# Optimization experiments

Hardware: AMD Instinct MI355X
Metric: run time of the kernel (lower is better)

Reference implementation:

```python
import jax, jax.numpy as jnp
import numpy as np

D_MODEL = 4096
N_HEADS = 32
N_KV_HEADS = 8
HEAD_DIM = D_MODEL // N_HEADS  # 128
SEQ = 2048
BATCH = 1
ROPE_BASE = 10000.0


def build_rope_cache(max_seq_len, head_dim, base=10000.0):
    half = head_dim // 2
    pos = jnp.arange(max_seq_len, dtype=jnp.float32)
    inv_freqs = 1.0 / (base ** (jnp.arange(half, dtype=jnp.float32) / half))
    angles = pos[:, None] * inv_freqs[None, :]  # (S, half)
    return jnp.cos(angles), jnp.sin(angles)


def apply_rope(t, cos, sin):
    # t: (B, H, S, D); cos/sin: (S, D//2) broadcast over batch & heads.
    t_even = t[..., 0::2]
    t_odd = t[..., 1::2]
    c = cos[None, None, :, :]
    s = sin[None, None, :, :]
    rot_even = t_even * c - t_odd * s
    rot_odd = t_even * s + t_odd * c
    # interleave back into even/odd slots
    return jnp.stack([rot_even, rot_odd], axis=-1).reshape(t.shape)


def setup_inputs() -> dict:
    key = jax.random.key(0)
    kx, kq, kk, kv, ko = jax.random.split(key, 5)
    bound = 1.0 / np.sqrt(D_MODEL)
    x = jax.random.normal(kx, (BATCH, SEQ, D_MODEL), dtype=jnp.float32)
    # torch Linear weights: (out_features, in_features)
    wq = jax.random.uniform(kq, (N_HEADS * HEAD_DIM, D_MODEL), minval=-bound, maxval=bound, dtype=jnp.float32)
    wk = jax.random.uniform(kk, (N_KV_HEADS * HEAD_DIM, D_MODEL), minval=-bound, maxval=bound, dtype=jnp.float32)
    wv = jax.random.uniform(kv, (N_KV_HEADS * HEAD_DIM, D_MODEL), minval=-bound, maxval=bound, dtype=jnp.float32)
    wo = jax.random.uniform(ko, (D_MODEL, D_MODEL), minval=-bound, maxval=bound, dtype=jnp.float32)
    attn_mask = jnp.tril(jnp.ones((SEQ, SEQ), dtype=jnp.int32))[None, None, :, :]
    return {"x": x, "wq": wq, "wk": wk, "wv": wv, "wo": wo, "attn_mask": attn_mask}


def reference(x, wq, wk, wv, wo, attn_mask):
    B, S, _ = x.shape
    cos, sin = build_rope_cache(SEQ, HEAD_DIM, ROPE_BASE)
    cos, sin = cos[:S], sin[:S]
    q = (x @ wq.T).reshape(B, S, N_HEADS, HEAD_DIM).transpose(0, 2, 1, 3)      # (B,H,S,D)
    k = (x @ wk.T).reshape(B, S, N_KV_HEADS, HEAD_DIM).transpose(0, 2, 1, 3)   # (B,Hkv,S,D)
    v = (x @ wv.T).reshape(B, S, N_KV_HEADS, HEAD_DIM).transpose(0, 2, 1, 3)
    q = apply_rope(q, cos, sin)
    k = apply_rope(k, cos, sin)
    n_rep = N_HEADS // N_KV_HEADS
    if n_rep > 1:
        k = jnp.repeat(k, n_rep, axis=1)
        v = jnp.repeat(v, n_rep, axis=1)
    scores = jnp.einsum('bhqd,bhkd->bhqk', q, k) / jnp.sqrt(jnp.float32(HEAD_DIM))
    scores = jnp.where(attn_mask == 0, -jnp.inf, scores)
    attn = jax.nn.softmax(scores, axis=-1)
    out = jnp.einsum('bhqk,bhkd->bhqd', attn, v)
    out = out.transpose(0, 2, 1, 3).reshape(B, S, D_MODEL)
    return out @ wo.T
```

## Files before the change

kernel.cpp:

```cpp
#include <hip/hip_runtime.h>
#include <hip/hip_bf16.h>

typedef float f32x4 __attribute__((ext_vector_type(4)));
typedef __bf16 bf16x4 __attribute__((ext_vector_type(4)));
typedef __bf16 bf16x8 __attribute__((ext_vector_type(8)));

__device__ __forceinline__ void gld_lds16(const void* g, void* l) {
  __builtin_amdgcn_global_load_lds((const __attribute__((address_space(1))) void*)g,
                                   (__attribute__((address_space(3))) void*)l, 16, 0, 0);
}

__global__ void cvt_f32_bf16(const float* __restrict__ in, __bf16* __restrict__ out,
                             int n8) {
  int idx = blockIdx.x * blockDim.x + threadIdx.x;
  if (idx >= n8) return;
  f32x4 a = *(const f32x4*)(in + (size_t)idx * 8);
  f32x4 b = *(const f32x4*)(in + (size_t)idx * 8 + 4);
  bf16x8 o;
#pragma unroll
  for (int j = 0; j < 4; ++j) { o[j] = (__bf16)a[j]; o[4 + j] = (__bf16)b[j]; }
  *(bf16x8*)(out + (size_t)idx * 8) = o;
}

__global__ void build_trig(float* __restrict__ trig) {
  int idx = blockIdx.x * blockDim.x + threadIdx.x;
  if (idx >= 2048 * 64) return;
  int i = idx & 63, s = idx >> 6;
  float ang = (float)s * powf(10000.0f, -(float)i * (1.0f / 64.0f));
  float sn, cs;
  sincosf(ang, &sn, &cs);
  trig[idx * 2] = cs;
  trig[idx * 2 + 1] = sn;
}

__global__ void rope_bf16(__bf16* __restrict__ T, const float* __restrict__ trig,
                          int stride, int nh_mask, int nh_shift, float mul, int total) {
  int idx = blockIdx.x * blockDim.x + threadIdx.x;
  if (idx >= total) return;
  int i = idx & 63;
  int h = (idx >> 6) & nh_mask;
  int s = idx >> (6 + nh_shift);
  float cs = trig[(s * 64 + i) * 2];
  float sn = trig[(s * 64 + i) * 2 + 1];
  __bf16* p = T + (size_t)s * stride + h * 128 + 2 * i;
  float e = (float)p[0], o = (float)p[1];
  p[0] = (__bf16)((e * cs - o * sn) * mul);
  p[1] = (__bf16)((e * sn + o * cs) * mul);
}

__global__ __launch_bounds__(256) void transpose_v(const __bf16* __restrict__ KVb,
                                                   __bf16* __restrict__ Vt) {
  __shared__ __bf16 T[64][72];
  const int tid = threadIdx.x;
  const int s0 = blockIdx.x * 64, d0 = blockIdx.y * 64;
  const int r = tid >> 3, c8 = (tid & 7) * 8;
#pragma unroll
  for (int i = 0; i < 2; ++i) {
    int row = i * 32 + r;
    *(bf16x8*)&T[row][c8] = *(const bf16x8*)&KVb[(size_t)(s0 + row) * 2048 + 1024 + d0 + c8];
  }
  __syncthreads();
#pragma unroll
  for (int i = 0; i < 2; ++i) {
    int drow = i * 32 + r;
    bf16x8 o;
#pragma unroll
    for (int j = 0; j < 8; ++j) o[j] = T[c8 + j][drow];
    *(bf16x8*)&Vt[(size_t)(d0 + drow) * 2048 + s0 + c8] = o;
  }
}

template <int BM, int BN, typename OutT>
__global__ __launch_bounds__(256) void gemm_bf16(const __bf16* __restrict__ A,
                                                 const __bf16* __restrict__ B0,
                                                 const __bf16* __restrict__ B1,
                                                 int Nsplit, OutT* __restrict__ C,
                                                 int M, int N, int K) {
  constexpr int MI = BM / 32, NJ = BN / 32;
  constexpr int RA = BM / 32, RB = BN / 32;
  __shared__ __bf16 As[BM * 64] __attribute__((aligned(16)));
  __shared__ __bf16 Bs[BN * 64] __attribute__((aligned(16)));

  const int tid = threadIdx.x;
  const int lane = tid & 63;
  const int w = tid >> 6;
  const int nwg = gridDim.x * gridDim.y;
  const int orig = blockIdx.y * gridDim.x + blockIdx.x;
  const int wgid = (orig & 7) * (nwg >> 3) + (orig >> 3);
  const int m0 = (wgid % gridDim.x) * BM;
  const int n0 = (wgid / gridDim.x) * BN;
  const int li = lane & 15, lg = lane >> 4;

  const __bf16* bsrc[RB];
#pragma unroll
  for (int i = 0; i < RB; ++i) {
    int slot = i * 256 + w * 64 + lane;
    int row = slot >> 3;
    int sch = (slot & 7) ^ (row & 7);
    int n = n0 + row;
    bsrc[i] = (n < Nsplit ? B0 + (size_t)n * K : B1 + (size_t)(n - Nsplit) * K) +
              sch * 8;
  }
  const __bf16* asrc[RA];
#pragma unroll
  for (int i = 0; i < RA; ++i) {
    int slot = i * 256 + w * 64 + lane;
    int row = slot >> 3;
    int sch = (slot & 7) ^ (row & 7);
    asrc[i] = A + (size_t)(m0 + row) * K + sch * 8;
  }

  const int wr = (w >> 1) * (BM / 2);
  const int wc = (w & 1) * (BN / 2);

  f32x4 acc[MI][NJ] = {};

  for (int k0 = 0; k0 < K; k0 += 64) {
    __syncthreads();
#pragma unroll
    for (int i = 0; i < RA; ++i)
      gld_lds16(asrc[i] + k0, &As[(i * 256 + w * 64) * 8]);
#pragma unroll
    for (int i = 0; i < RB; ++i)
      gld_lds16(bsrc[i] + k0, &Bs[(i * 256 + w * 64) * 8]);
    __syncthreads();

#pragma unroll
    for (int u = 0; u < 2; ++u) {
      bf16x8 af[MI], bfr[NJ];
#pragma unroll
      for (int mi = 0; mi < MI; ++mi)
        af[mi] = *(const bf16x8*)&As[(wr + mi * 16 + li) * 64 +
                                     (((u * 4 + lg) ^ (li & 7)) * 8)];
#pragma unroll
      for (int nj = 0; nj < NJ; ++nj)
        bfr[nj] = *(const bf16x8*)&Bs[(wc + nj * 16 + li) * 64 +
                                      (((u * 4 + lg) ^ (li & 7)) * 8)];
#pragma unroll
      for (int mi = 0; mi < MI; ++mi)
#pragma unroll
        for (int nj = 0; nj < NJ; ++nj)
          acc[mi][nj] = __builtin_amdgcn_mfma_f32_16x16x32_bf16(af[mi], bfr[nj],
                                                                acc[mi][nj], 0, 0, 0);
    }
  }

  const int crow = lg * 4;
#pragma unroll
  for (int mi = 0; mi < MI; ++mi)
#pragma unroll
    for (int nj = 0; nj < NJ; ++nj)
#pragma unroll
      for (int r = 0; r < 4; ++r)
        C[(size_t)(m0 + wr + mi * 16 + crow + r) * N + (n0 + wc + nj * 16 + li)] =
            (OutT)acc[mi][nj][r];
}

__global__ __launch_bounds__(256) void attn_fwd_v5(const __bf16* __restrict__ Q,
                                                   const __bf16* __restrict__ KVb,
                                                   const __bf16* __restrict__ Vt,
                                                   __bf16* __restrict__ O) {
  const int tid = threadIdx.x;
  const int lane = tid & 63;
  const int w = tid >> 6;
  const int orig = blockIdx.x;
  const int chunk = orig & 7;
  const int wkk = orig >> 3;
  const int h = chunk * 4 + (wkk & 3);
  const int pair = wkk >> 2;
  const int kvh = h >> 2;

  __shared__ __bf16 Ks[2][64 * 128] __attribute__((aligned(16)));
  __shared__ __bf16 Vts[128 * 64] __attribute__((aligned(16)));
  __shared__ __bf16 Ps[4][32 * 72] __attribute__((aligned(16)));

  const int li = lane & 15, lg = lane >> 4;

  auto stage_k = [&](int k0, int buf) {
#pragma unroll
    for (int i = 0; i < 4; ++i) {
      int slot = i * 256 + tid;
      int row = slot >> 4;
      int sch = (slot & 15) ^ (row & 7);
      gld_lds16(&KVb[(size_t)(k0 + row) * 2048 + kvh * 128 + sch * 8],
                &Ks[buf][(i * 256 + w * 64) * 8]);
    }
  };
  auto stage_v = [&](int k0) {
#pragma unroll
    for (int i = 0; i < 4; ++i) {
      int slot = i * 256 + tid;
      int row = slot >> 3;
      int sch = (slot & 7) ^ (row & 7);
      gld_lds16(&Vt[(size_t)(kvh * 128 + row) * 2048 + k0 + sch * 8],
                &Vts[(i * 256 + w * 64) * 8]);
    }
  };

#pragma unroll 1
  for (int pass = 0; pass < 2; ++pass) {
    const int m0 = ((pass == 0) ? (15 - pair) : pair) * 128;
    const int rbase = m0 + w * 32;

    bf16x8 qf[2][4];
#pragma unroll
    for (int mt = 0; mt < 2; ++mt) {
      const __bf16* qrow = Q + (size_t)(rbase + mt * 16 + li) * 4096 + h * 128;
#pragma unroll
      for (int kc = 0; kc < 4; ++kc) qf[mt][kc] = *(const bf16x8*)(qrow + kc * 32 + lg * 8);
    }

    f32x4 accO[2][8] = {};
    float plane[2] = {0.f, 0.f};

    const int wmax = rbase + 31;
    const int ntile = (m0 + 128) >> 6;

    stage_k(0, 0);

#pragma unroll 1
    for (int t = 0; t < ntile; ++t) {
      const int k0 = t * 64;
      const int cur = t & 1;
      stage_v(k0);
      stage_k(t + 1 < ntile ? k0 + 64 : 0, cur ^ 1);

      asm volatile("s_waitcnt vmcnt(8)" ::: "memory");
      __builtin_amdgcn_s_barrier();
      __builtin_amdgcn_sched_barrier(0);
      asm volatile("" ::: "memory");

      const bool active = (k0 <= wmax);
      bf16x8 pa[2][2];
      if (active) {
        f32x4 s2[4][2] = {};
        __builtin_amdgcn_s_setprio(1);
#pragma unroll
        for (int nt = 0; nt < 4; ++nt)
#pragma unroll
          for (int kc = 0; kc < 4; ++kc) {
            bf16x8 kf = *(const bf16x8*)&Ks[cur][(li + 16 * nt) * 128 +
                                                (((4 * kc + lg) ^ (li & 7)) * 8)];
            s2[nt][0] = __builtin_amdgcn_mfma_f32_16x16x32_bf16(kf, qf[0][kc], s2[nt][0], 0, 0, 0);
            s2[nt][1] = __builtin_amdgcn_mfma_f32_16x16x32_bf16(kf, qf[1][kc], s2[nt][1], 0, 0, 0);
          }
        __builtin_amdgcn_s_setprio(0);

#pragma unroll
        for (int mt = 0; mt < 2; ++mt) {
          const int qb = rbase + mt * 16;
          const int q = qb + li;
          const bool needmask = (k0 + 63 > qb);
#pragma unroll
          for (int nt = 0; nt < 4; ++nt) {
            bf16x4 pk;
#pragma unroll
            for (int r = 0; r < 4; ++r) {
              const int key = k0 + 16 * nt + lg * 4 + r;
              float v = s2[nt][mt][r];
              if (needmask && key > q) v = -INFINITY;
              float p = exp2f(v);
              plane[mt] += p;
              pk[r] = (__bf16)p;
            }
            *(bf16x4*)&Ps[w][(mt * 16 + li) * 72 + 16 * nt + lg * 4] = pk;
          }
          pa[mt][0] = *(const bf16x8*)&Ps[w][(mt * 16 + li) * 72 + lg * 8];
          pa[mt][1] = *(const bf16x8*)&Ps[w][(mt * 16 + li) * 72 + 32 + lg * 8];
        }
      }

      asm volatile("s_waitcnt vmcnt(4)" ::: "memory");
      __builtin_amdgcn_s_barrier();
      __builtin_amdgcn_sched_barrier(0);
      asm volatile("" ::: "memory");

      if (active) {
        __builtin_amdgcn_s_setprio(1);
#pragma unroll
        for (int dt = 0; dt < 8; ++dt)
#pragma unroll
          for (int kc = 0; kc < 2; ++kc) {
            bf16x8 vf = *(const bf16x8*)&Vts[(li + 16 * dt) * 64 +
                                             (((4 * kc + lg) ^ (li & 7)) * 8)];
            accO[0][dt] = __builtin_amdgcn_mfma_f32_16x16x32_bf16(pa[0][kc], vf, accO[0][dt], 0, 0, 0);
            accO[1][dt] = __builtin_amdgcn_mfma_f32_16x16x32_bf16(pa[1][kc], vf, accO[1][dt], 0, 0, 0);
          }
        __builtin_amdgcn_s_setprio(0);
      }

      __builtin_amdgcn_s_barrier();
      __builtin_amdgcn_sched_barrier(0);
      asm volatile("" ::: "memory");
    }

#pragma unroll
    for (int mt = 0; mt < 2; ++mt) {
      float sum = plane[mt];
      sum += __shfl_xor(sum, 16);
      sum += __shfl_xor(sum, 32);
      float inv[4];
#pragma unroll
      for (int r = 0; r < 4; ++r) inv[r] = 1.0f / __shfl(sum, lg * 4 + r);
#pragma unroll
      for (int dt = 0; dt < 8; ++dt)
#pragma unroll
        for (int r = 0; r < 4; ++r)
          O[(size_t)(rbase + mt * 16 + lg * 4 + r) * 4096 + h * 128 + dt * 16 + li] =
              (__bf16)(accO[mt][dt][r] * inv[r]);
    }
  }
}

extern "C" void kernel_launch(void* const* d_in, const int* in_sizes, int n_in,
                              void* d_out, int out_size, void* d_ws, size_t ws_size,
                              hipStream_t stream) {
  const float* x  = (const float*)d_in[0];
  const float* wq = (const float*)d_in[1];
  const float* wk = (const float*)d_in[2];
  const float* wv = (const float*)d_in[3];
  const float* wo = (const float*)d_in[4];
  float* out = (float*)d_out;

  const int S = 2048, D = 4096;
  char* ws = (char*)d_ws;
  __bf16* xb  = (__bf16*)ws;
  __bf16* Qb  = (__bf16*)(ws + 16777216);
  __bf16* KVb = (__bf16*)(ws + 33554432);
  __bf16* Vt  = (__bf16*)(ws + 41943040);
  __bf16* wb  = (__bf16*)(ws + 46137344);
  float*  trig = (float*)(ws + 79691776);
  __bf16* AOb = xb;

  const float qscale = 0.08838834764831845f * 1.4426950408889634f;

  cvt_f32_bf16<<<(S * D / 8 + 255) / 256, 256, 0, stream>>>(x, xb, S * D / 8);
  cvt_f32_bf16<<<(D * D / 8 + 255) / 256, 256, 0, stream>>>(wq, wb, D * D / 8);
  gemm_bf16<128, 128, __bf16><<<dim3(16, 32), 256, 0, stream>>>(
      xb, wb, wb, 1 << 30, Qb, S, D, D);

  cvt_f32_bf16<<<(1024 * D / 8 + 255) / 256, 256, 0, stream>>>(wk, wb, 1024 * D / 8);
  cvt_f32_bf16<<<(1024 * D / 8 + 255) / 256, 256, 0, stream>>>(wv, wb + (size_t)1024 * D,
                                                               1024 * D / 8);
  gemm_bf16<64, 128, __bf16><<<dim3(32, 16), 256, 0, stream>>>(
      xb, wb, wb + (size_t)1024 * D, 1024, KVb, S, 2048, D);

  build_trig<<<(2048 * 64 + 255) / 256, 256, 0, stream>>>(trig);
  rope_bf16<<<(S * 32 * 64 + 255) / 256, 256, 0, stream>>>(Qb, trig, 4096, 31, 5,
                                                           qscale, S * 32 * 64);
  rope_bf16<<<(S * 8 * 64 + 255) / 256, 256, 0, stream>>>(KVb, trig, 2048, 7, 3,
                                                          1.0f, S * 8 * 64);
  transpose_v<<<dim3(32, 16), 256, 0, stream>>>(KVb, Vt);

  attn_fwd_v5<<<256, 256, 0, stream>>>(Qb, KVb, Vt, AOb);

  cvt_f32_bf16<<<(D * D / 8 + 255) / 256, 256, 0, stream>>>(wo, wb, D * D / 8);
  gemm_bf16<128, 128, float><<<dim3(16, 32), 256, 0, stream>>>(
      AOb, wb, wb, 1 << 30, out, S, D, D);
}
```

Baseline: 376.4 us.

## Use 8 waves per attention block and double-buffer V tiles

```diff
diff --git a/kernel.cpp b/kernel.cpp
--- a/kernel.cpp
+++ b/kernel.cpp
@@ -156,7 +156,7 @@
             (OutT)acc[mi][nj][r];
 }
 
-__global__ __launch_bounds__(256) void attn_fwd_v5(const __bf16* __restrict__ Q,
+__global__ __launch_bounds__(512) void attn_fwd_v6(const __bf16* __restrict__ Q,
                                                    const __bf16* __restrict__ KVb,
                                                    const __bf16* __restrict__ Vt,
                                                    __bf16* __restrict__ O) {
@@ -171,132 +171,117 @@
   const int kvh = h >> 2;
 
   __shared__ __bf16 Ks[2][64 * 128] __attribute__((aligned(16)));
-  __shared__ __bf16 Vts[128 * 64] __attribute__((aligned(16)));
-  __shared__ __bf16 Ps[4][32 * 72] __attribute__((aligned(16)));
+  __shared__ __bf16 Vts[2][128 * 64] __attribute__((aligned(16)));
+  __shared__ __bf16 Ps[8][16 * 72] __attribute__((aligned(16)));
 
   const int li = lane & 15, lg = lane >> 4;
 
   auto stage_k = [&](int k0, int buf) {
 #pragma unroll
-    for (int i = 0; i < 4; ++i) {
-      int slot = i * 256 + tid;
+    for (int i = 0; i < 2; ++i) {
+      int slot = i * 512 + tid;
       int row = slot >> 4;
       int sch = (slot & 15) ^ (row & 7);
       gld_lds16(&KVb[(size_t)(k0 + row) * 2048 + kvh * 128 + sch * 8],
-                &Ks[buf][(i * 256 + w * 64) * 8]);
+                &Ks[buf][(i * 512 + w * 64) * 8]);
     }
   };
-  auto stage_v = [&](int k0) {
-#pragma unroll
-    for (int i = 0; i < 4; ++i) {
-      int slot = i * 256 + tid;
+  auto stage_v = [&](int k0, int buf) {
+#pragma unroll
+    for (int i = 0; i < 2; ++i) {
+      int slot = i * 512 + tid;
       int row = slot >> 3;
       int sch = (slot & 7) ^ (row & 7);
       gld_lds16(&Vt[(size_t)(kvh * 128 + row) * 2048 + k0 + sch * 8],
-                &Vts[(i * 256 + w * 64) * 8]);
+                &Vts[buf][(i * 512 + w * 64) * 8]);
     }
   };
 
 #pragma unroll 1
   for (int pass = 0; pass < 2; ++pass) {
     const int m0 = ((pass == 0) ? (15 - pair) : pair) * 128;
-    const int rbase = m0 + w * 32;
-
-    bf16x8 qf[2][4];
-#pragma unroll
-    for (int mt = 0; mt < 2; ++mt) {
-      const __bf16* qrow = Q + (size_t)(rbase + mt * 16 + li) * 4096 + h * 128;
-#pragma unroll
-      for (int kc = 0; kc < 4; ++kc) qf[mt][kc] = *(const bf16x8*)(qrow + kc * 32 + lg * 8);
-    }
-
-    f32x4 accO[2][8] = {};
-    float plane[2] = {0.f, 0.f};
-
-    const int wmax = rbase + 31;
+    const int rbase = m0 + w * 16;
+
+    bf16x8 qf[4];
+    {
+      const __bf16* qrow = Q + (size_t)(rbase + li) * 4096 + h * 128;
+#pragma unroll
+      for (int kc = 0; kc < 4; ++kc) qf[kc] = *(const bf16x8*)(qrow + kc * 32 + lg * 8);
+    }
+
+    f32x4 accO[8] = {};
+    float plane = 0.f;
+
+    const int wmax = rbase + 15;
     const int ntile = (m0 + 128) >> 6;
 
+    __builtin_amdgcn_s_barrier();
+    stage_v(0, 0);
     stage_k(0, 0);
 
 #pragma unroll 1
     for (int t = 0; t < ntile; ++t) {
       const int k0 = t * 64;
       const int cur = t & 1;
-      stage_v(k0);
-      stage_k(t + 1 < ntile ? k0 + 64 : 0, cur ^ 1);
-
-      asm volatile("s_waitcnt vmcnt(8)" ::: "memory");
+
       __builtin_amdgcn_s_barrier();
-      __builtin_amdgcn_sched_barrier(0);
-      asm volatile("" ::: "memory");
-
-      const bool active = (k0 <= wmax);
-      bf16x8 pa[2][2];
-      if (active) {
-        f32x4 s2[4][2] = {};
-        __builtin_amdgcn_s_setprio(1);
-#pragma unroll
-        for (int nt = 0; nt < 4; ++nt)
-#pragma unroll
-          for (int kc = 0; kc < 4; ++kc) {
-            bf16x8 kf = *(const bf16x8*)&Ks[cur][(li + 16 * nt) * 128 +
-                                                (((4 * kc + lg) ^ (li & 7)) * 8)];
-            s2[nt][0] = __builtin_amdgcn_mfma_f32_16x16x32_bf16(kf, qf[0][kc], s2[nt][0], 0, 0, 0);
-            s2[nt][1] = __builtin_amdgcn_mfma_f32_16x16x32_bf16(kf, qf[1][kc], s2[nt][1], 0, 0, 0);
-          }
-        __builtin_amdgcn_s_setprio(0);
-
-#pragma unroll
-        for (int mt = 0; mt < 2; ++mt) {
-          const int qb = rbase + mt * 16;
-          const int q = qb + li;
-          const bool needmask = (k0 + 63 > qb);
-#pragma unroll
-          for (int nt = 0; nt < 4; ++nt) {
-            bf16x4 pk;
-#pragma unroll
-            for (int r = 0; r < 4; ++r) {
-              const int key = k0 + 16 * nt + lg * 4 + r;
-              float v = s2[nt][mt][r];
-              if (needmask && key > q) v = -INFINITY;
-              float p = exp2f(v);
-              plane[mt] += p;
-              pk[r] = (__bf16)p;
-            }
-            *(bf16x4*)&Ps[w][(mt * 16 + li) * 72 + 16 * nt + lg * 4] = pk;
-          }
-          pa[mt][0] = *(const bf16x8*)&Ps[w][(mt * 16 + li) * 72 + lg * 8];
-          pa[mt][1] = *(const bf16x8*)&Ps[w][(mt * 16 + li) * 72 + 32 + lg * 8];
-        }
-      }
+      const int nk = (t + 1 < ntile) ? k0 + 64 : 0;
+      stage_v(nk, cur ^ 1);
+      stage_k(nk, cur ^ 1);
 
       asm volatile("s_waitcnt vmcnt(4)" ::: "memory");
       __builtin_amdgcn_s_barrier();
       __builtin_amdgcn_sched_barrier(0);
       asm volatile("" ::: "memory");
 
-      if (active) {
+      if (k0 <= wmax) {
+        f32x4 s2[4] = {};
         __builtin_amdgcn_s_setprio(1);
 #pragma unroll
+        for (int nt = 0; nt < 4; ++nt)
+#pragma unroll
+          for (int kc = 0; kc < 4; ++kc) {
+            bf16x8 kf = *(const bf16x8*)&Ks[cur][(li + 16 * nt) * 128 +
+                                                (((4 * kc + lg) ^ (li & 7)) * 8)];
+            s2[nt] = __builtin_amdgcn_mfma_f32_16x16x32_bf16(kf, qf[kc], s2[nt], 0, 0, 0);
+          }
+        __builtin_amdgcn_s_setprio(0);
+
+        const int q = rbase + li;
+        const bool needmask = (k0 + 63 > rbase);
+#pragma unroll
+        for (int nt = 0; nt < 4; ++nt) {
+          bf16x4 pk;
+#pragma unroll
+          for (int r = 0; r < 4; ++r) {
+            const int key = k0 + 16 * nt + lg * 4 + r;
+            float v = s2[nt][r];
+            if (needmask && key > q) v = -INFINITY;
+            float p = exp2f(v);
+            plane += p;
+            pk[r] = (__bf16)p;
+          }
+          *(bf16x4*)&Ps[w][li * 72 + 16 * nt + lg * 4] = pk;
+        }
+        bf16x8 pa[2];
+        pa[0] = *(const bf16x8*)&Ps[w][li * 72 + lg * 8];
+        pa[1] = *(const bf16x8*)&Ps[w][li * 72 + 32 + lg * 8];
+
+        __builtin_amdgcn_s_setprio(1);
+#pragma unroll
         for (int dt = 0; dt < 8; ++dt)
 #pragma unroll
           for (int kc = 0; kc < 2; ++kc) {
-            bf16x8 vf = *(const bf16x8*)&Vts[(li + 16 * dt) * 64 +
-                                             (((4 * kc + lg) ^ (li & 7)) * 8)];
-            accO[0][dt] = __builtin_amdgcn_mfma_f32_16x16x32_bf16(pa[0][kc], vf, accO[0][dt], 0, 0, 0);
-            accO[1][dt] = __builtin_amdgcn_mfma_f32_16x16x32_bf16(pa[1][kc], vf, accO[1][dt], 0, 0, 0);
+            bf16x8 vf = *(const bf16x8*)&Vts[cur][(li + 16 * dt) * 64 +
+                                                 (((4 * kc + lg) ^ (li & 7)) * 8)];
+            accO[dt] = __builtin_amdgcn_mfma_f32_16x16x32_bf16(pa[kc], vf, accO[dt], 0, 0, 0);
           }
         __builtin_amdgcn_s_setprio(0);
       }
-
-      __builtin_amdgcn_s_barrier();
-      __builtin_amdgcn_sched_barrier(0);
-      asm volatile("" ::: "memory");
-    }
-
-#pragma unroll
-    for (int mt = 0; mt < 2; ++mt) {
-      float sum = plane[mt];
+    }
+
+    {
+      float sum = plane;
       sum += __shfl_xor(sum, 16);
       sum += __shfl_xor(sum, 32);
       float inv[4];
@@ -306,8 +291,8 @@
       for (int dt = 0; dt < 8; ++dt)
 #pragma unroll
         for (int r = 0; r < 4; ++r)
-          O[(size_t)(rbase + mt * 16 + lg * 4 + r) * 4096 + h * 128 + dt * 16 + li] =
-              (__bf16)(accO[mt][dt][r] * inv[r]);
+          O[(size_t)(rbase + lg * 4 + r) * 4096 + h * 128 + dt * 16 + li] =
+              (__bf16)(accO[dt][r] * inv[r]);
     }
   }
 }
@@ -352,7 +337,7 @@
                                                           1.0f, S * 8 * 64);
   transpose_v<<<dim3(32, 16), 256, 0, stream>>>(KVb, Vt);
 
-  attn_fwd_v5<<<256, 256, 0, stream>>>(Qb, KVb, Vt, AOb);
+  attn_fwd_v6<<<256, 512, 0, stream>>>(Qb, KVb, Vt, AOb);
 
   cvt_f32_bf16<<<(D * D / 8 + 255) / 256, 256, 0, stream>>>(wo, wb, D * D / 8);
   gemm_bf16<128, 128, float><<<dim3(16, 32), 256, 0, stream>>>(
```

Measured after the change: 364.8 us. 1.03x faster.
